# Kernel tuning notes

Measured on AMD Instinct MI355X. Metric: run time of the kernel, lower is better.

## Reference

```python
import jax, jax.numpy as jnp
import numpy as np

T, B, IN, H = 256, 64, 512, 1024

def setup_inputs() -> dict:
    key = jax.random.key(0)
    ks = jax.random.split(key, 8)
    s_in = 1.0 / np.sqrt(IN)
    s_h = 1.0 / np.sqrt(H)
    return {
        "inp": jax.random.normal(ks[0], (T, B, IN), jnp.float32),
        "img": jax.random.normal(ks[1], (B, H), jnp.float32),
        "Wxh": jax.random.uniform(ks[2], (4 * H, IN), jnp.float32, -s_in, s_in),
        "bxh": jax.random.uniform(ks[3], (4 * H,), jnp.float32, -s_in, s_in),
        "Whh": jax.random.uniform(ks[4], (4 * H, H), jnp.float32, -s_h, s_h),
        "bhh": jax.random.uniform(ks[5], (4 * H,), jnp.float32, -s_h, s_h),
        "Wout": jax.random.uniform(ks[6], (IN, H), jnp.float32, -s_h, s_h),
        "bout": jax.random.uniform(ks[7], (IN,), jnp.float32, -s_h, s_h),
    }

def reference(inp, img, Wxh, bxh, Whh, bhh, Wout, bout):
    t_len, b, _ = inp.shape
    h_dim = Whh.shape[1]
    img4 = jnp.concatenate([img, img, img, img], axis=1)  # [B, 4H]
    # precompute input projection for all timesteps: [T, B, 4H]
    xproj = jnp.einsum('tbi,gi->tbg', inp, Wxh) + bxh
    xproj = xproj.at[0].add(img4)

    def step(carry, xg):
        h, c = carry
        gates = xg + h @ Whh.T + bhh  # [B, 4H]
        i_g, f_g, g_g, o_g = jnp.split(gates, 4, axis=1)
        c = jax.nn.sigmoid(f_g) * c + jax.nn.sigmoid(i_g) * jnp.tanh(g_g)
        h = jax.nn.sigmoid(o_g) * jnp.tanh(c)
        return (h, c), h

    zeros = jnp.zeros((b, h_dim), inp.dtype)
    _, hs = jax.lax.scan(step, (zeros, zeros), xproj)  # hs: [T, B, H]
    out = jnp.einsum('tbh,vh->tbv', hs, Wout) + bout  # [T, B, IN]
    return jax.nn.log_softmax(out, axis=-1)
```

## Files before the change

### kernel.cpp

```cpp
#include <hip/hip_runtime.h>
#include <math.h>

#define T_LEN 256
#define B_SZ  64
#define IN_D  512
#define H_D   1024
#define G4    4096

typedef float  f32x4 __attribute__((ext_vector_type(4)));
typedef short  s16x8 __attribute__((ext_vector_type(8)));
typedef unsigned short u16;
typedef unsigned int   u32;

__device__ __forceinline__ void gl_lds16(const void* g, void* l) {
  __builtin_amdgcn_global_load_lds(
      (const __attribute__((address_space(1))) unsigned int*)g,
      (__attribute__((address_space(3))) unsigned int*)l, 16, 0, 0);
}

__device__ __forceinline__ u16 f2bf(float f) {
  union { float f; unsigned u; } v; v.f = f;
  unsigned x = v.u;
  unsigned r = (x + 0x7fffu + ((x >> 16) & 1u)) >> 16;
  return (u16)r;
}
__device__ __forceinline__ float bf2f(u16 b) {
  union { unsigned u; float f; } v; v.u = ((unsigned)b) << 16;
  return v.f;
}
__device__ __forceinline__ float sigm(float x) {
  return 1.0f / (1.0f + __expf(-x));
}

__global__ void cvt_f32_bf16(const float* __restrict__ src, u16* __restrict__ dst, int n) {
  int i = blockIdx.x * blockDim.x + threadIdx.x;
  int stride = gridDim.x * blockDim.x;
  for (; i < n; i += stride) dst[i] = f2bf(src[i]);
}

template<int KD, int EPI>
__launch_bounds__(256)
__global__ void gemm_bt(const u16* __restrict__ A, const u16* __restrict__ Bm,
                        const float* __restrict__ bias, const float* __restrict__ img,
                        u16* __restrict__ Cb, float* __restrict__ Cf, int Ncols) {
  __shared__ u16 sA[128 * 64];
  __shared__ u16 sB[128 * 64];
  const int tid  = threadIdx.x;
  const int wave = tid >> 6, lane = tid & 63;
  const int wm = wave >> 1, wn = wave & 1;
  const int mBase = blockIdx.y * 128;
  const int nBase = blockIdx.x * 128;

  f32x4 acc[4][4] = {};

  for (int k0 = 0; k0 < KD; k0 += 64) {
#pragma unroll
    for (int it = 0; it < 4; ++it) {
      int s = it * 256 + tid;
      int row = s >> 3, c = s & 7;
      int gc = c ^ (row & 7);
      const u16* ga = A  + (size_t)(mBase + row) * KD + k0 + gc * 8;
      const u16* gb = Bm + (size_t)(nBase + row) * KD + k0 + gc * 8;
      gl_lds16(ga, &sA[(it * 256 + wave * 64) * 8]);
      gl_lds16(gb, &sB[(it * 256 + wave * 64) * 8]);
    }
    __syncthreads();

    const int q = lane >> 4, rl = lane & 15;
#pragma unroll
    for (int ks = 0; ks < 64; ks += 32) {
      s16x8 af[4], bfr[4];
      int gcb = (ks >> 3) + q;
#pragma unroll
      for (int i = 0; i < 4; ++i) {
        int rowA = wm * 64 + i * 16 + rl;
        af[i]  = *(const s16x8*)&sA[rowA * 64 + (gcb ^ (rowA & 7)) * 8];
        int rowB = wn * 64 + i * 16 + rl;
        bfr[i] = *(const s16x8*)&sB[rowB * 64 + (gcb ^ (rowB & 7)) * 8];
      }
#pragma unroll
      for (int i = 0; i < 4; ++i)
#pragma unroll
        for (int j = 0; j < 4; ++j)
          acc[i][j] = __builtin_amdgcn_mfma_f32_16x16x32_bf16(af[i], bfr[j], acc[i][j], 0, 0, 0);
    }
    __syncthreads();
  }

#pragma unroll
  for (int i = 0; i < 4; ++i) {
    int rbase = mBase + wm * 64 + i * 16 + ((lane >> 4) << 2);
#pragma unroll
    for (int j = 0; j < 4; ++j) {
      int col = nBase + wn * 64 + j * 16 + (lane & 15);
      float bc = bias[col];
#pragma unroll
      for (int r = 0; r < 4; ++r) {
        int row = rbase + r;
        float v = acc[i][j][r] + bc;
        if (EPI == 0) {
          if (row < B_SZ) v += img[row * H_D + (col & (H_D - 1))];
          Cb[(size_t)row * Ncols + col] = f2bf(v);
        } else {
          Cf[(size_t)row * Ncols + col] = v;
        }
      }
    }
  }
}

#define WPAD 1032
__launch_bounds__(256, 1)
__global__ void lstm_rec(const u16* __restrict__ WhhB, const u16* __restrict__ xproj,
                         const float* __restrict__ bhh, u32* __restrict__ hs32,
                         int* __restrict__ flags) {
  __shared__ u16  sW[64 * WPAD];
  __shared__ u16  sH[16 * 512];
  __shared__ float sG[4][16][16];

  const int tid  = threadIdx.x;
  const int wave = tid >> 6, lane = tid & 63;
  const int grp = blockIdx.x >> 6;
  const int wg  = blockIdx.x & 63;
  const int bBase = grp * 16;
  const int colBase = wg * 16;

  for (int it = 0; it < 32; ++it) {
    int s = it * 256 + tid;
    int n = s >> 7, c = s & 127;
    int grow = (n >> 4) * H_D + colBase + (n & 15);
    s16x8 v = *(const s16x8*)(WhhB + (size_t)grow * H_D + c * 8);
    *(s16x8*)&sW[n * WPAD + c * 8] = v;
  }
  __syncthreads();

  float cst = 0.f;
  const int ub = tid >> 4, uc = tid & 15;
  const int gb = bBase + ub;
  const int gcol = colBase + uc;
  const float bh_i = bhh[0 * H_D + gcol], bh_f = bhh[1 * H_D + gcol];
  const float bh_g = bhh[2 * H_D + gcol], bh_o = bhh[3 * H_D + gcol];
  const int q = lane >> 4, rl = lane & 15;

  for (int t = 0; t < T_LEN; ++t) {
    const u16* xp = xproj + ((size_t)t * B_SZ + gb) * G4;
    float gi_ = bf2f(xp[0 * H_D + gcol]) + bh_i;
    float gf_ = bf2f(xp[1 * H_D + gcol]) + bh_f;
    float gg_ = bf2f(xp[2 * H_D + gcol]) + bh_g;
    float go_ = bf2f(xp[3 * H_D + gcol]) + bh_o;

    if (t > 0) {
      if (tid < 64) {
        const int* fp = flags + (t - 1) * 256 + grp * 64 + tid;
        while (__hip_atomic_load(fp, __ATOMIC_RELAXED, __HIP_MEMORY_SCOPE_AGENT) == 0)
          __builtin_amdgcn_s_sleep(1);
      }
      __syncthreads();

      u32 v[32];
      const u32* hp = hs32 + (size_t)(t - 1) * B_SZ * 512 + (size_t)bBase * 512;
#pragma unroll
      for (int j = 0; j < 32; ++j) {
        int d = j * 256 + tid;
        v[j] = __hip_atomic_load(&hp[(d >> 9) * 512 + (d & 511)],
                                 __ATOMIC_RELAXED, __HIP_MEMORY_SCOPE_AGENT);
      }

      f32x4 acc = {0.f, 0.f, 0.f, 0.f};
#pragma unroll
      for (int half = 0; half < 2; ++half) {
        int chunk = tid >> 2;
        int off = (tid & 3) * 2;
#pragma unroll
        for (int r = 0; r < 16; ++r)
          *(u32*)&sH[r * 512 + ((chunk ^ (r & 7)) * 8 + off)] = v[2 * r + half];
        __syncthreads();
#pragma unroll
        for (int ks = 0; ks < 512; ks += 32) {
          int gc = (ks >> 3) + q;
          s16x8 afr = *(const s16x8*)&sH[rl * 512 + ((gc ^ (rl & 7)) & 63) * 8];
          s16x8 bfr = *(const s16x8*)&sW[(wave * 16 + rl) * WPAD + half * 512 + ks + q * 8];
          acc = __builtin_amdgcn_mfma_f32_16x16x32_bf16(afr, bfr, acc, 0, 0, 0);
        }
        __syncthreads();
      }
#pragma unroll
      for (int r = 0; r < 4; ++r)
        sG[wave][(lane >> 4) * 4 + r][lane & 15] = acc[r];
      __syncthreads();
      gi_ += sG[0][ub][uc]; gf_ += sG[1][ub][uc];
      gg_ += sG[2][ub][uc]; go_ += sG[3][ub][uc];
      __syncthreads();
    }

    cst = sigm(gf_) * cst + sigm(gi_) * tanhf(gg_);
    float h = sigm(go_) * tanhf(cst);
    u32 bits = f2bf(h);
    u32 partner = (u32)__shfl_xor((int)bits, 1);
    if ((tid & 1) == 0) {
      __hip_atomic_store(&hs32[((size_t)t * B_SZ + gb) * 512 + (gcol >> 1)],
                         bits | (partner << 16),
                         __ATOMIC_RELAXED, __HIP_MEMORY_SCOPE_AGENT);
    }
    __builtin_amdgcn_s_waitcnt(0);
    __syncthreads();
    if (tid == 0)
      __hip_atomic_store(&flags[t * 256 + grp * 64 + wg], 1,
                         __ATOMIC_RELAXED, __HIP_MEMORY_SCOPE_AGENT);
  }
}

__launch_bounds__(256)
__global__ void logsoftmax_rows(float* __restrict__ out) {
  __shared__ float red[8];
  float* p = out + (size_t)blockIdx.x * IN_D;
  const int tid = threadIdx.x;
  float v0 = p[tid], v1 = p[tid + 256];
  float m = fmaxf(v0, v1);
#pragma unroll
  for (int off = 32; off > 0; off >>= 1) m = fmaxf(m, __shfl_down(m, off));
  if ((tid & 63) == 0) red[tid >> 6] = m;
  __syncthreads();
  m = fmaxf(fmaxf(red[0], red[1]), fmaxf(red[2], red[3]));
  float e = __expf(v0 - m) + __expf(v1 - m);
#pragma unroll
  for (int off = 32; off > 0; off >>= 1) e += __shfl_down(e, off);
  if ((tid & 63) == 0) red[4 + (tid >> 6)] = e;
  __syncthreads();
  float ls = m + logf(red[4] + red[5] + red[6] + red[7]);
  p[tid] = v0 - ls;
  p[tid + 256] = v1 - ls;
}

extern "C" void kernel_launch(void* const* d_in, const int* in_sizes, int n_in,
                              void* d_out, int out_size, void* d_ws, size_t ws_size,
                              hipStream_t stream) {
  const float* inp  = (const float*)d_in[0];
  const float* img  = (const float*)d_in[1];
  const float* Wxh  = (const float*)d_in[2];
  const float* bxh  = (const float*)d_in[3];
  const float* Whh  = (const float*)d_in[4];
  const float* bhh  = (const float*)d_in[5];
  const float* Wout = (const float*)d_in[6];
  const float* bout = (const float*)d_in[7];
  float* out = (float*)d_out;

  char* ws = (char*)d_ws;
  u16* inpB   = (u16*)(ws);
  u16* WxhB   = (u16*)(ws + 16777216);
  u16* WhhB   = (u16*)(ws + 20971520);
  u16* WoutB  = (u16*)(ws + 29360128);
  u16* xprojB = (u16*)(ws + 30408704);
  u16* hsB    = (u16*)(ws + 164626432);
  int* flags  = (int*)(ws + 198180864);

  cvt_f32_bf16<<<2048, 256, 0, stream>>>(inp,  inpB,  T_LEN * B_SZ * IN_D);
  cvt_f32_bf16<<<2048, 256, 0, stream>>>(Wxh,  WxhB,  G4 * IN_D);
  cvt_f32_bf16<<<2048, 256, 0, stream>>>(Whh,  WhhB,  G4 * H_D);
  cvt_f32_bf16<<<2048, 256, 0, stream>>>(Wout, WoutB, IN_D * H_D);
  hipMemsetAsync(flags, 0, T_LEN * 256 * sizeof(int), stream);

  gemm_bt<IN_D, 0><<<dim3(G4 / 128, 16384 / 128), 256, 0, stream>>>(
      inpB, WxhB, bxh, img, xprojB, nullptr, G4);

  lstm_rec<<<256, 256, 0, stream>>>(WhhB, xprojB, bhh, (u32*)hsB, flags);

  gemm_bt<H_D, 1><<<dim3(IN_D / 128, 16384 / 128), 256, 0, stream>>>(
      hsB, WoutB, bout, nullptr, nullptr, out, IN_D);

  logsoftmax_rows<<<16384, 256, 0, stream>>>(out);
}
```

Baseline: 1.195 ms.

## Keep Whh slice in registers, split K across waves, vectorize h exchange

The recurrent kernel now holds each wave's slice of Whh for all four gates in registers (32 bf16x8 fragments) instead of LDS. Each wave covers a quarter of the K dimension for all gates, and the four partial sums are reduced through a padded LDS buffer. This drops the two-half LDS staging loop and its extra barriers. The previous h is loaded with dwordx4 sc1 loads and stored as packed dwordx4 after shuffles, and tanh is replaced with an exp-based formula. The cost is much higher register pressure and a slightly less accurate tanh.

Result: faster. 1.077 ms (-9.9%).

```diff
diff --git a/kernel.cpp b/kernel.cpp
--- a/kernel.cpp
+++ b/kernel.cpp
@@ -9,6 +9,7 @@
 
 typedef float  f32x4 __attribute__((ext_vector_type(4)));
 typedef short  s16x8 __attribute__((ext_vector_type(8)));
+typedef unsigned int u32x4 __attribute__((ext_vector_type(4)));
 typedef unsigned short u16;
 typedef unsigned int   u32;
 
@@ -30,6 +31,10 @@
 }
 __device__ __forceinline__ float sigm(float x) {
   return 1.0f / (1.0f + __expf(-x));
+}
+__device__ __forceinline__ float tanh_f(float x) {
+  float e = __expf(2.0f * x);
+  return 1.0f - 2.0f / (e + 1.0f);
 }
 
 __global__ void cvt_f32_bf16(const float* __restrict__ src, u16* __restrict__ dst, int n) {
@@ -109,14 +114,12 @@
   }
 }
 
-#define WPAD 1032
 __launch_bounds__(256, 1)
 __global__ void lstm_rec(const u16* __restrict__ WhhB, const u16* __restrict__ xproj,
                          const float* __restrict__ bhh, u32* __restrict__ hs32,
                          int* __restrict__ flags) {
-  __shared__ u16  sW[64 * WPAD];
-  __shared__ u16  sH[16 * 512];
-  __shared__ float sG[4][16][16];
+  __shared__ u16  sH[16 * 1024];
+  __shared__ float sGp[16][16][17];
 
   const int tid  = threadIdx.x;
   const int wave = tid >> 6, lane = tid & 63;
@@ -124,15 +127,17 @@
   const int wg  = blockIdx.x & 63;
   const int bBase = grp * 16;
   const int colBase = wg * 16;
-
-  for (int it = 0; it < 32; ++it) {
-    int s = it * 256 + tid;
-    int n = s >> 7, c = s & 127;
-    int grow = (n >> 4) * H_D + colBase + (n & 15);
-    s16x8 v = *(const s16x8*)(WhhB + (size_t)grow * H_D + c * 8);
-    *(s16x8*)&sW[n * WPAD + c * 8] = v;
-  }
-  __syncthreads();
+  const int q = lane >> 4, rl = lane & 15;
+
+  s16x8 wf[4][8];
+  {
+    const u16* wb = WhhB + (size_t)(colBase + rl) * H_D + wave * 256 + q * 8;
+#pragma unroll
+    for (int g = 0; g < 4; ++g)
+#pragma unroll
+      for (int m = 0; m < 8; ++m)
+        wf[g][m] = *(const s16x8*)(wb + (size_t)g * H_D * H_D + m * 32);
+  }
 
   float cst = 0.f;
   const int ub = tid >> 4, uc = tid & 15;
@@ -140,7 +145,6 @@
   const int gcol = colBase + uc;
   const float bh_i = bhh[0 * H_D + gcol], bh_f = bhh[1 * H_D + gcol];
   const float bh_g = bhh[2 * H_D + gcol], bh_o = bhh[3 * H_D + gcol];
-  const int q = lane >> 4, rl = lane & 15;
 
   for (int t = 0; t < T_LEN; ++t) {
     const u16* xp = xproj + ((size_t)t * B_SZ + gb) * G4;
@@ -157,50 +161,63 @@
       }
       __syncthreads();
 
-      u32 v[32];
+      u32x4 v[8];
       const u32* hp = hs32 + (size_t)(t - 1) * B_SZ * 512 + (size_t)bBase * 512;
 #pragma unroll
-      for (int j = 0; j < 32; ++j) {
-        int d = j * 256 + tid;
-        v[j] = __hip_atomic_load(&hp[(d >> 9) * 512 + (d & 511)],
-                                 __ATOMIC_RELAXED, __HIP_MEMORY_SCOPE_AGENT);
-      }
-
-      f32x4 acc = {0.f, 0.f, 0.f, 0.f};
-#pragma unroll
-      for (int half = 0; half < 2; ++half) {
-        int chunk = tid >> 2;
-        int off = (tid & 3) * 2;
-#pragma unroll
-        for (int r = 0; r < 16; ++r)
-          *(u32*)&sH[r * 512 + ((chunk ^ (r & 7)) * 8 + off)] = v[2 * r + half];
-        __syncthreads();
-#pragma unroll
-        for (int ks = 0; ks < 512; ks += 32) {
-          int gc = (ks >> 3) + q;
-          s16x8 afr = *(const s16x8*)&sH[rl * 512 + ((gc ^ (rl & 7)) & 63) * 8];
-          s16x8 bfr = *(const s16x8*)&sW[(wave * 16 + rl) * WPAD + half * 512 + ks + q * 8];
-          acc = __builtin_amdgcn_mfma_f32_16x16x32_bf16(afr, bfr, acc, 0, 0, 0);
-        }
-        __syncthreads();
-      }
-#pragma unroll
-      for (int r = 0; r < 4; ++r)
-        sG[wave][(lane >> 4) * 4 + r][lane & 15] = acc[r];
+      for (int j = 0; j < 8; ++j) {
+        int cid = j * 256 + tid;
+        const u32* p = hp + (cid >> 7) * 512 + (cid & 127) * 4;
+        asm volatile("global_load_dwordx4 %0, %1, off sc1"
+                     : "=v"(v[j]) : "v"(p) : "memory");
+      }
+      asm volatile("s_waitcnt vmcnt(0)" ::: "memory");
+#pragma unroll
+      for (int j = 0; j < 8; ++j) {
+        int cid = j * 256 + tid;
+        int r = cid >> 7, c = cid & 127;
+        *(s16x8*)&sH[r * 1024 + (c ^ (r & 7)) * 8] = *(s16x8*)&v[j];
+      }
       __syncthreads();
-      gi_ += sG[0][ub][uc]; gf_ += sG[1][ub][uc];
-      gg_ += sG[2][ub][uc]; go_ += sG[3][ub][uc];
+
+      f32x4 a0 = {}, a1 = {}, a2 = {}, a3 = {};
+#pragma unroll
+      for (int m = 0; m < 8; ++m) {
+        int chunk = wave * 32 + m * 4 + q;
+        s16x8 afr = *(const s16x8*)&sH[rl * 1024 + ((chunk ^ (rl & 7))) * 8];
+        a0 = __builtin_amdgcn_mfma_f32_16x16x32_bf16(afr, wf[0][m], a0, 0, 0, 0);
+        a1 = __builtin_amdgcn_mfma_f32_16x16x32_bf16(afr, wf[1][m], a1, 0, 0, 0);
+        a2 = __builtin_amdgcn_mfma_f32_16x16x32_bf16(afr, wf[2][m], a2, 0, 0, 0);
+        a3 = __builtin_amdgcn_mfma_f32_16x16x32_bf16(afr, wf[3][m], a3, 0, 0, 0);
+      }
+#pragma unroll
+      for (int r = 0; r < 4; ++r) {
+        int row = (lane >> 4) * 4 + r;
+        sGp[wave * 4 + 0][row][lane & 15] = a0[r];
+        sGp[wave * 4 + 1][row][lane & 15] = a1[r];
+        sGp[wave * 4 + 2][row][lane & 15] = a2[r];
+        sGp[wave * 4 + 3][row][lane & 15] = a3[r];
+      }
       __syncthreads();
-    }
-
-    cst = sigm(gf_) * cst + sigm(gi_) * tanhf(gg_);
-    float h = sigm(go_) * tanhf(cst);
-    u32 bits = f2bf(h);
-    u32 partner = (u32)__shfl_xor((int)bits, 1);
-    if ((tid & 1) == 0) {
-      __hip_atomic_store(&hs32[((size_t)t * B_SZ + gb) * 512 + (gcol >> 1)],
-                         bits | (partner << 16),
-                         __ATOMIC_RELAXED, __HIP_MEMORY_SCOPE_AGENT);
+      gi_ += sGp[0][ub][uc] + sGp[4][ub][uc] + sGp[8][ub][uc]  + sGp[12][ub][uc];
+      gf_ += sGp[1][ub][uc] + sGp[5][ub][uc] + sGp[9][ub][uc]  + sGp[13][ub][uc];
+      gg_ += sGp[2][ub][uc] + sGp[6][ub][uc] + sGp[10][ub][uc] + sGp[14][ub][uc];
+      go_ += sGp[3][ub][uc] + sGp[7][ub][uc] + sGp[11][ub][uc] + sGp[15][ub][uc];
+    }
+
+    cst = sigm(gf_) * cst + sigm(gi_) * tanh_f(gg_);
+    float h = sigm(go_) * tanh_f(cst);
+
+    u32 b = f2bf(h);
+    u32 p1 = (u32)__shfl_xor((int)b, 1);
+    u32 w0 = b | (p1 << 16);
+    u32 w1 = (u32)__shfl_xor((int)w0, 2);
+    u32 w2 = (u32)__shfl_xor((int)w0, 4);
+    u32 w3 = (u32)__shfl_xor((int)w1, 4);
+    if ((tid & 7) == 0) {
+      u32x4 pk = {w0, w1, w2, w3};
+      u32* dst = hs32 + ((size_t)t * B_SZ + gb) * 512 + (gcol >> 1);
+      asm volatile("global_store_dwordx4 %0, %1, off sc1"
+                   :: "v"(dst), "v"(pk) : "memory");
     }
     __builtin_amdgcn_s_waitcnt(0);
     __syncthreads();
```
